# Kernel optimization log

Hardware: AMD Instinct MI355X
Metric: run time of the kernel (lower is better)

The kernel has to match this reference:

```python
import jax, jax.numpy as jnp
import numpy as np

B_SZ, SEQ = 1, 2048
D_MODEL, D_STATE, D_CONV, EXPAND = 768, 64, 4, 2
D_INNER = EXPAND * D_MODEL            # 1536
HEADDIM = 64
NHEADS = D_INNER // HEADDIM           # 24
CONV_DIM = D_INNER + 2 * D_STATE      # 1664
D_IN_PROJ = 2 * D_INNER + 2 * D_STATE + NHEADS  # 3224
HIDDEN = ((D_MODEL * EXPAND + 127) // 128) * 128  # 1536
EPS = 1e-5


def _ln(x, w, b):
    m = x.mean(-1, keepdims=True)
    v = ((x - m) ** 2).mean(-1, keepdims=True)
    return (x - m) * jax.lax.rsqrt(v + EPS) * w + b


def setup_inputs() -> dict:
    key = jax.random.key(0)
    ks = jax.random.split(key, 8)
    s = 0.02
    return {
        "x": jax.random.normal(ks[0], (B_SZ, SEQ, D_MODEL), jnp.float32),
        "ln1_w": jnp.ones((D_MODEL,), jnp.float32),
        "ln1_b": jnp.zeros((D_MODEL,), jnp.float32),
        "ln2_w": jnp.ones((D_MODEL,), jnp.float32),
        "ln2_b": jnp.zeros((D_MODEL,), jnp.float32),
        "in_proj_w": jax.random.normal(ks[1], (D_IN_PROJ, D_MODEL), jnp.float32) * s,
        "conv_w": jax.random.normal(ks[2], (CONV_DIM, D_CONV), jnp.float32) * s,
        "conv_b": jnp.zeros((CONV_DIM,), jnp.float32),
        "dt_bias": jax.random.normal(ks[3], (NHEADS,), jnp.float32) * 0.1,
        "A_log": jnp.log(jax.random.uniform(ks[4], (NHEADS,), jnp.float32, 1.0, 16.0)),
        "D_skip": jnp.ones((NHEADS,), jnp.float32),
        "ssm_norm_w": jnp.ones((D_INNER,), jnp.float32),
        "out_proj_w": jax.random.normal(ks[5], (D_MODEL, D_INNER), jnp.float32) * s,
        "fc1_w": jax.random.normal(ks[6], (2 * HIDDEN, D_MODEL), jnp.float32) * s,
        "fc2_w": jax.random.normal(ks[7], (D_MODEL, HIDDEN), jnp.float32) * s,
    }


def _block(x, ln1_w, ln1_b, ln2_w, ln2_b, in_proj_w, conv_w, conv_b,
           dt_bias, A_log, D_skip, ssm_norm_w, out_proj_w, fc1_w, fc2_w):
    Bb, L, _ = x.shape
    # --- Mamba2 SSM mixer ---
    h = _ln(x, ln1_w, ln1_b)
    zxbcdt = jnp.einsum('bld,pd->blp', h, in_proj_w)  # (B,L,D_IN_PROJ)
    z = zxbcdt[..., :D_INNER]
    xBC = zxbcdt[..., D_INNER:D_INNER + CONV_DIM]
    dt = zxbcdt[..., D_INNER + CONV_DIM:]             # (B,L,NHEADS)
    # causal depthwise conv1d (kernel D_CONV)
    xp = jnp.pad(xBC, ((0, 0), (D_CONV - 1, 0), (0, 0)))
    xBC = sum(xp[:, k:k + L, :] * conv_w[:, k] for k in range(D_CONV)) + conv_b
    xBC = jax.nn.silu(xBC)
    xs = xBC[..., :D_INNER].reshape(Bb, L, NHEADS, HEADDIM)
    Bm = xBC[..., D_INNER:D_INNER + D_STATE]          # (B,L,N) ngroups=1
    Cm = xBC[..., D_INNER + D_STATE:]                 # (B,L,N)
    dt = jax.nn.softplus(dt + dt_bias)                # (B,L,H)
    dA = jnp.exp(dt * (-jnp.exp(A_log)))              # (B,L,H)
    dtx = dt[..., None] * xs                          # (B,L,H,P)

    def step(hprev, inp):
        dA_t, dtx_t, B_t, C_t = inp
        hn = hprev * dA_t[:, :, None, None] + dtx_t[..., None] * B_t[:, None, None, :]
        return hn, jnp.einsum('bhps,bs->bhp', hn, C_t)

    h0 = jnp.zeros((Bb, NHEADS, HEADDIM, D_STATE), x.dtype)
    _, ys = jax.lax.scan(step, h0, (dA.swapaxes(0, 1), dtx.swapaxes(0, 1),
                                    Bm.swapaxes(0, 1), Cm.swapaxes(0, 1)))
    y = ys.swapaxes(0, 1) + D_skip[None, None, :, None] * xs  # (B,L,H,P)
    y = y.reshape(Bb, L, D_INNER) * jax.nn.silu(z)
    # gated RMSNorm
    y = y * jax.lax.rsqrt((y * y).mean(-1, keepdims=True) + EPS) * ssm_norm_w
    x = x + jnp.einsum('bli,di->bld', y, out_proj_w)
    # --- Gated MLP ---
    h2 = _ln(x, ln2_w, ln2_b)
    f = jnp.einsum('bld,hd->blh', h2, fc1_w)
    f = f[..., :HIDDEN] * jax.nn.silu(f[..., HIDDEN:])
    return x + jnp.einsum('blh,dh->bld', f, fc2_w)


def reference(x, ln1_w, ln1_b, ln2_w, ln2_b, in_proj_w, conv_w, conv_b,
              dt_bias, A_log, D_skip, ssm_norm_w, out_proj_w, fc1_w, fc2_w):
    return _block(x, ln1_w, ln1_b, ln2_w, ln2_b, in_proj_w, conv_w, conv_b,
                  dt_bias, A_log, D_skip, ssm_norm_w, out_proj_w, fc1_w, fc2_w)
```

## Files before the change

### kernel.cpp

```cpp
#include <hip/hip_runtime.h>
#include <math.h>

#define D_MODEL 768
#define SEQ 2048
#define D_STATE 64
#define D_CONV 4
#define D_INNER 1536
#define HEADDIM 64
#define NHEADS 24
#define CONV_DIM 1664
#define D_IN_PROJ 3224
#define HIDDEN 1536
#define EPS 1e-5f
#define NCHUNK 32
#define CHUNK 64

typedef short s16x8 __attribute__((ext_vector_type(8)));
typedef float f32x4 __attribute__((ext_vector_type(4)));

#define SWZ(row, k) (((row) << 6) + ((((k) >> 3) ^ ((row) & 7)) << 3) + ((k) & 7))

__device__ __forceinline__ float silu_f(float x) { return x / (1.f + expf(-x)); }

__device__ __forceinline__ short f2bf(float x) {
  unsigned u = __builtin_bit_cast(unsigned, x);
  unsigned r = (u + 0x7fffu + ((u >> 16) & 1u)) >> 16;
  return (short)r;
}
__device__ __forceinline__ float bf2f(short s) {
  unsigned u = ((unsigned)(unsigned short)s) << 16;
  return __builtin_bit_cast(float, u);
}

__device__ __forceinline__ float block_sum256(float v, float* sdata) {
#pragma unroll
  for (int o = 32; o > 0; o >>= 1) v += __shfl_down(v, o);
  int lane = threadIdx.x & 63, wid = threadIdx.x >> 6;
  __syncthreads();
  if (lane == 0) sdata[wid] = v;
  __syncthreads();
  if (threadIdx.x == 0) sdata[0] = sdata[0] + sdata[1] + sdata[2] + sdata[3];
  __syncthreads();
  return sdata[0];
}

__device__ __forceinline__ void gll16(const short* gsrc, const short* ldst) {
  __builtin_amdgcn_global_load_lds(
      (const __attribute__((address_space(1))) unsigned int*)(unsigned long long)gsrc,
      (__attribute__((address_space(3))) unsigned int*)(unsigned int)(unsigned long long)ldst,
      16, 0, 0);
}

__device__ __forceinline__ void ln_row(const float* __restrict__ xr,
                                       const float* __restrict__ w,
                                       const float* __restrict__ b,
                                       short* __restrict__ orow, float* red) {
  float v[3];
#pragma unroll
  for (int k = 0; k < 3; k++) v[k] = xr[threadIdx.x + k * 256];
  float s = v[0] + v[1] + v[2];
  s = block_sum256(s, red);
  float mean = s * (1.f / 768.f);
  float q = 0.f;
#pragma unroll
  for (int k = 0; k < 3; k++) { float d = v[k] - mean; q += d * d; }
  q = block_sum256(q, red);
  float rstd = rsqrtf(q * (1.f / 768.f) + EPS);
#pragma unroll
  for (int k = 0; k < 3; k++) {
    int i = threadIdx.x + k * 256;
    orow[i] = f2bf((v[k] - mean) * rstd * w[i] + b[i]);
  }
}

__global__ __launch_bounds__(256) void ln_kernel(const float* __restrict__ x,
                                                 const float* __restrict__ w,
                                                 const float* __restrict__ b,
                                                 short* __restrict__ out) {
  __shared__ float red[8];
  int row = blockIdx.x;
  ln_row(x + (size_t)row * D_MODEL, w, b, out + (size_t)row * D_MODEL, red);
}

#define T_WINP (3328 * 768)
#define R_WINP (3224 * 768)
#define T_FC1 (3072 * 768)
#define T_W768 (1536 * 768)
__global__ __launch_bounds__(256) void cast_ln_kernel(
    const float* __restrict__ x, const float* __restrict__ ln1w,
    const float* __restrict__ ln1b, short* __restrict__ hbf,
    const float* __restrict__ Win, const float* __restrict__ Wfc1,
    const float* __restrict__ Wout, const float* __restrict__ Wfc2,
    short* __restrict__ WA, short* __restrict__ WF1,
    short* __restrict__ WB, short* __restrict__ WC) {
  __shared__ float red[8];
  if (blockIdx.x < SEQ) {
    int row = blockIdx.x;
    ln_row(x + (size_t)row * D_MODEL, ln1w, ln1b, hbf + (size_t)row * D_MODEL, red);
    return;
  }
  int idx = (blockIdx.x - SEQ) * 256 + threadIdx.x;
  if (idx < T_WINP) {
    WA[idx] = (idx < R_WINP) ? f2bf(Win[idx]) : (short)0;
    return;
  }
  idx -= T_WINP;
  if (idx < T_FC1) {
    int np = idx / 768, k = idx % 768;
    int srow = (np & 1) ? (HIDDEN + (np >> 1)) : (np >> 1);
    WF1[idx] = f2bf(Wfc1[(size_t)srow * 768 + k]);
    return;
  }
  idx -= T_FC1;
  if (idx < T_W768) { WB[idx] = f2bf(Wout[idx]); return; }
  idx -= T_W768;
  if (idx < T_W768) WC[idx] = f2bf(Wfc2[idx]);
}

template <int MREP, int NREP, int CHUNKMODE, int OMODE>
__global__ __launch_bounds__(256) void mfma_gemm_bt(const short* __restrict__ A,
                                                    const short* __restrict__ Bw,
                                                    void* __restrict__ Cout,
                                                    const float* __restrict__ res,
                                                    int GX, int GY, int Nreal, int K) {
  constexpr int BMr = MREP * 32;
  constexpr int BNr = NREP * 32;
  __shared__ short As[BMr * 64];
  __shared__ short Bs[BNr * 64];
  int tid = threadIdx.x, w = tid >> 6, l = tid & 63;
  int per8 = gridDim.x >> 3;
  int L = (blockIdx.x & 7) * per8 + (blockIdx.x >> 3);
  int xt, yt;
  if constexpr (CHUNKMODE == 0) { xt = L / GY; yt = L - xt * GY; }
  else                          { yt = L / GX; xt = L - yt * GX; }
  int m0 = yt * BMr, n0 = xt * BNr;
  int wr = (w >> 1) * (MREP * 16), wc = (w & 1) * (NREP * 16);
  f32x4 acc[MREP][NREP] = {};

  for (int kt = 0; kt < K; kt += 64) {
    __syncthreads();
#pragma unroll
    for (int q = 0; q < BMr / 32; q++) {
      int chunk = w * (BMr / 32) + q;
      int rr = chunk * 8 + (l >> 3);
      int gs = (l & 7) ^ (rr & 7);
      gll16(A + (size_t)(m0 + rr) * K + kt + gs * 8, As + chunk * 512);
    }
#pragma unroll
    for (int q = 0; q < BNr / 32; q++) {
      int chunk = w * (BNr / 32) + q;
      int rr = chunk * 8 + (l >> 3);
      int gs = (l & 7) ^ (rr & 7);
      gll16(Bw + (size_t)(n0 + rr) * K + kt + gs * 8, Bs + chunk * 512);
    }
    __syncthreads();
#pragma unroll
    for (int half = 0; half < 2; half++) {
      s16x8 af[MREP], bfr[NREP];
      int kk = half * 32 + (l >> 4) * 8;
#pragma unroll
      for (int mi = 0; mi < MREP; mi++)
        af[mi] = *(const s16x8*)&As[SWZ(wr + mi * 16 + (l & 15), kk)];
#pragma unroll
      for (int nj = 0; nj < NREP; nj++)
        bfr[nj] = *(const s16x8*)&Bs[SWZ(wc + nj * 16 + (l & 15), kk)];
#pragma unroll
      for (int mi = 0; mi < MREP; mi++)
#pragma unroll
        for (int nj = 0; nj < NREP; nj++)
          acc[mi][nj] = __builtin_amdgcn_mfma_f32_16x16x32_bf16(af[mi], bfr[nj],
                                                                acc[mi][nj], 0, 0, 0);
    }
  }
#pragma unroll
  for (int mi = 0; mi < MREP; mi++)
#pragma unroll
    for (int nj = 0; nj < NREP; nj++)
#pragma unroll
      for (int r = 0; r < 4; r++) {
        int mm = m0 + wr + mi * 16 + (l >> 4) * 4 + r;
        int nn = n0 + wc + nj * 16 + (l & 15);
        float v = acc[mi][nj][r];
        if constexpr (OMODE == 0) {
          float* C = (float*)Cout;
          if (nn < Nreal) {
            if (res) v += res[(size_t)mm * Nreal + nn];
            C[(size_t)mm * Nreal + nn] = v;
          }
        } else if constexpr (OMODE == 1) {
          short* C = (short*)Cout;
          if (nn < Nreal) C[(size_t)mm * Nreal + nn] = f2bf(v);
        } else {
          float pv = __shfl_xor(v, 1);
          if ((l & 1) == 0) {
            short* g = (short*)Cout;
            g[(size_t)mm * (Nreal >> 1) + (nn >> 1)] = f2bf(v * silu_f(pv));
          }
        }
      }
}

__global__ __launch_bounds__(256) void conv_pack_kernel(const short* __restrict__ zx,
                                                        const float* __restrict__ cw,
                                                        const float* __restrict__ cb,
                                                        const float* __restrict__ dtb,
                                                        const float* __restrict__ Alog,
                                                        short* __restrict__ xsb,
                                                        short* __restrict__ XTall,
                                                        short* __restrict__ BTg,
                                                        short* __restrict__ BCbf,
                                                        float* __restrict__ dts,
                                                        float* __restrict__ laB) {
  int ct = blockIdx.x, rt = blockIdx.y;
  if (ct == 26) {
    int wv = threadIdx.x >> 6, t = threadIdx.x & 63;
    int gt = rt * 64 + t;
#pragma unroll
    for (int i = 0; i < 6; i++) {
      int h = wv * 6 + i;
      float xv = bf2f(zx[(size_t)gt * D_IN_PROJ + 3200 + h]) + dtb[h];
      float sp = (xv > 20.f) ? xv : log1pf(expf(xv));
      float la = -expf(Alog[h]) * sp;
#pragma unroll
      for (int off = 1; off < 64; off <<= 1) {
        float u = __shfl_up(la, off);
        if (t >= off) la += u;
      }
      dts[gt * NHEADS + h] = sp;
      laB[gt * NHEADS + h] = la;
    }
    return;
  }
  __shared__ float T[64][65];
  int lane = threadIdx.x & 63, grp = threadIdx.x >> 6;
  int c = ct * 64 + lane;
  float4 w4 = *(const float4*)&cw[c * 4];
  float cbv = cb[c];
  int t0 = rt * 64 + grp * 16;
  float vbuf[19];
#pragma unroll
  for (int jj = 0; jj < 19; jj++) {
    int tt = t0 + jj - 3;
    vbuf[jj] = (tt >= 0) ? bf2f(zx[(size_t)tt * D_IN_PROJ + D_INNER + c]) : 0.f;
  }
#pragma unroll
  for (int j = 0; j < 16; j++) {
    float acc = cbv + vbuf[j] * w4.x + vbuf[j + 1] * w4.y +
                vbuf[j + 2] * w4.z + vbuf[j + 3] * w4.w;
    float v = silu_f(acc);
    int row = grp * 16 + j;
    T[row][lane] = v;
    if (ct < 24)
      xsb[(size_t)(rt * 64 + row) * D_INNER + c] = f2bf(v);
    else
      BCbf[(size_t)(rt * 64 + row) * 128 + (ct - 24) * 64 + lane] = f2bf(v);
  }
  __syncthreads();
  if (ct < 24) {
#pragma unroll
    for (int j = 0; j < 16; j++) {
      int cc = grp * 16 + j;
      XTall[(size_t)(ct * 64 + cc) * 2048 + rt * 64 + lane] = f2bf(T[lane][cc]);
    }
  } else if (ct == 24) {
#pragma unroll
    for (int j = 0; j < 16; j++) {
      int cc = grp * 16 + j;
      BTg[(size_t)cc * 2048 + rt * 64 + lane] = f2bf(T[lane][cc]);
    }
  }
}

__global__ __launch_bounds__(256) void ssd_a_kernel(const short* __restrict__ BCbf,
                                                    const short* __restrict__ XTall,
                                                    const short* __restrict__ BTg,
                                                    const float* __restrict__ laB,
                                                    const float* __restrict__ dts,
                                                    short* __restrict__ ylg,
                                                    short* __restrict__ Sbh) {
  __shared__ short Cl[4096], Bl[4096], XTl[4096], BTl[4096], Ml[4096];
  __shared__ float la_s[64], dt_s[64], w_s[64];
  int b = blockIdx.x;
  int c = b / NHEADS, h = b % NHEADS;
  int tid = threadIdx.x, w = tid >> 6, l = tid & 63;

  {
    const short* gC = BCbf + (size_t)(c * 64) * 128 + 64;
    const short* gB = BCbf + (size_t)(c * 64) * 128;
    const short* gX = XTall + (size_t)(h * 64) * 2048 + c * 64;
    const short* gT = BTg + c * 64;
#pragma unroll
    for (int q = 0; q < 2; q++) {
      int row = w * 16 + q * 8 + (l >> 3);
      int ks = (l & 7) ^ (row & 7);
      int lofs = (w * 16 + q * 8) * 64;
      gll16(gC + (size_t)row * 128 + ks * 8, Cl + lofs);
      gll16(gB + (size_t)row * 128 + ks * 8, Bl + lofs);
      gll16(gX + (size_t)row * 2048 + ks * 8, XTl + lofs);
      gll16(gT + (size_t)row * 2048 + ks * 8, BTl + lofs);
    }
  }
  if (tid < 64) {
    la_s[tid] = laB[(c * CHUNK + tid) * NHEADS + h];
    dt_s[tid] = dts[(c * CHUNK + tid) * NHEADS + h];
  }
  __syncthreads();

  f32x4 gacc[4] = {};
#pragma unroll
  for (int kt = 0; kt < 2; kt++) {
    int ar = w * 16 + (l & 15);
    int kk = kt * 32 + (l >> 4) * 8;
    s16x8 af = *(const s16x8*)&Cl[SWZ(ar, kk)];
#pragma unroll
    for (int nj = 0; nj < 4; nj++) {
      s16x8 bf_ = *(const s16x8*)&Bl[SWZ(nj * 16 + (l & 15), kk)];
      gacc[nj] = __builtin_amdgcn_mfma_f32_16x16x32_bf16(af, bf_, gacc[nj], 0, 0, 0);
    }
  }
  if (tid < 64) w_s[tid] = __expf(la_s[63] - la_s[tid]) * dt_s[tid];
#pragma unroll
  for (int nj = 0; nj < 4; nj++)
#pragma unroll
    for (int r = 0; r < 4; r++) {
      int t = w * 16 + (l >> 4) * 4 + r;
      int s = nj * 16 + (l & 15);
      float m = (s <= t) ? gacc[nj][r] * __expf(la_s[t] - la_s[s]) * dt_s[s] : 0.f;
      Ml[SWZ(t, s)] = f2bf(m);
    }
  __syncthreads();
  {
    int s = tid & 63, tg = (tid >> 6) * 16;
#pragma unroll
    for (int j = 0; j < 16; j++) {
      int t = tg + j;
      int a = SWZ(s, t);
      BTl[a] = f2bf(bf2f(BTl[a]) * w_s[t]);
    }
  }
  __syncthreads();

  f32x4 yacc[4] = {};
#pragma unroll
  for (int kt = 0; kt < 2; kt++) {
    int ar = w * 16 + (l & 15);
    int kk = kt * 32 + (l >> 4) * 8;
    s16x8 af = *(const s16x8*)&Ml[SWZ(ar, kk)];
#pragma unroll
    for (int nj = 0; nj < 4; nj++) {
      s16x8 bf_ = *(const s16x8*)&XTl[SWZ(nj * 16 + (l & 15), kk)];
      yacc[nj] = __builtin_amdgcn_mfma_f32_16x16x32_bf16(af, bf_, yacc[nj], 0, 0, 0);
    }
  }
  f32x4 hacc[4] = {};
#pragma unroll
  for (int kt = 0; kt < 2; kt++) {
    int ar = w * 16 + (l & 15);
    int kk = kt * 32 + (l >> 4) * 8;
    s16x8 af = *(const s16x8*)&XTl[SWZ(ar, kk)];
#pragma unroll
    for (int nj = 0; nj < 4; nj++) {
      s16x8 bf_ = *(const s16x8*)&BTl[SWZ(nj * 16 + (l & 15), kk)];
      hacc[nj] = __builtin_amdgcn_mfma_f32_16x16x32_bf16(af, bf_, hacc[nj], 0, 0, 0);
    }
  }
#pragma unroll
  for (int nj = 0; nj < 4; nj++)
#pragma unroll
    for (int r = 0; r < 4; r++) {
      int t = w * 16 + (l >> 4) * 4 + r;
      int p = nj * 16 + (l & 15);
      ylg[(size_t)(c * CHUNK + t) * D_INNER + h * 64 + p] = f2bf(yacc[nj][r]);
      Sbh[((size_t)(c * NHEADS + h) * 64 + t) * 64 + p] = f2bf(hacc[nj][r]);
    }
}

__global__ __launch_bounds__(256) void scan2_kernel(const short* __restrict__ Sbh,
                                                    const float* __restrict__ laB,
                                                    short* __restrict__ Hsbf) {
  int idx = blockIdx.x * 256 + threadIdx.x;
  int hh = idx >> 12;
  int rem = idx & 4095;
  float Sv[NCHUNK];
#pragma unroll
  for (int c = 0; c < NCHUNK; c++)
    Sv[c] = bf2f(Sbh[((size_t)c * NHEADS + hh) * 4096 + rem]);
  float run = 0.f;
#pragma unroll
  for (int c = 0; c < NCHUNK; c++) {
    float P = __expf(laB[(c * CHUNK + CHUNK - 1) * NHEADS + hh]);
    Hsbf[((size_t)c * NHEADS + hh) * 4096 + rem] = f2bf(run);
    run = fmaf(P, run, Sv[c]);
  }
}

__global__ __launch_bounds__(256) void ssd_b_kernel(const short* __restrict__ BCbf,
                                                    const short* __restrict__ Hsbf,
                                                    const float* __restrict__ laB,
                                                    const float* __restrict__ Dsk,
                                                    const short* __restrict__ xsb,
                                                    const short* __restrict__ zx,
                                                    short* __restrict__ ylg) {
  __shared__ short Cl[4096], Hl[4096];
  __shared__ float la_s[64];
  int b = blockIdx.x;
  int c = b / NHEADS, h = b % NHEADS;
  int tid = threadIdx.x, w = tid >> 6, l = tid & 63;
  {
    const short* gC = BCbf + (size_t)(c * 64) * 128 + 64;
    const short* gH = Hsbf + (size_t)(c * NHEADS + h) * 4096;
#pragma unroll
    for (int q = 0; q < 2; q++) {
      int row = w * 16 + q * 8 + (l >> 3);
      int ks = (l & 7) ^ (row & 7);
      int lofs = (w * 16 + q * 8) * 64;
      gll16(gC + (size_t)row * 128 + ks * 8, Cl + lofs);
      gll16(gH + (size_t)row * 64 + ks * 8, Hl + lofs);
    }
  }
  if (tid < 64) la_s[tid] = laB[(c * CHUNK + tid) * NHEADS + h];
  __syncthreads();
  f32x4 acc[4] = {};
#pragma unroll
  for (int kt = 0; kt < 2; kt++) {
    int ar = w * 16 + (l & 15);
    int kk = kt * 32 + (l >> 4) * 8;
    s16x8 af = *(const s16x8*)&Cl[SWZ(ar, kk)];
#pragma unroll
    for (int nj = 0; nj < 4; nj++) {
      s16x8 bf_ = *(const s16x8*)&Hl[SWZ(nj * 16 + (l & 15), kk)];
      acc[nj] = __builtin_amdgcn_mfma_f32_16x16x32_bf16(af, bf_, acc[nj], 0, 0, 0);
    }
  }
  float Dv = Dsk[h];
#pragma unroll
  for (int nj = 0; nj < 4; nj++)
#pragma unroll
    for (int r = 0; r < 4; r++) {
      int t = w * 16 + (l >> 4) * 4 + r;
      int p = nj * 16 + (l & 15);
      size_t gt = c * CHUNK + t;
      size_t gi = gt * D_INNER + h * 64 + p;
      float yv = bf2f(ylg[gi]) + acc[nj][r] * __expf(la_s[t]) +
                 Dv * bf2f(xsb[gt * D_INNER + h * 64 + p]);
      float z = bf2f(zx[gt * D_IN_PROJ + h * 64 + p]);
      ylg[gi] = f2bf(yv * silu_f(z));
    }
}

__global__ __launch_bounds__(256) void rmsnorm_bf_kernel(const short* __restrict__ g,
                                                         const float* __restrict__ nw,
                                                         short* __restrict__ ybn) {
  __shared__ float red[8];
  int t = blockIdx.x;
  const short* gr = g + (size_t)t * D_INNER;
  float v[6];
  float ss = 0.f;
#pragma unroll
  for (int k = 0; k < 6; k++) {
    v[k] = bf2f(gr[threadIdx.x + k * 256]);
    ss += v[k] * v[k];
  }
  ss = block_sum256(ss, red);
  float rs = rsqrtf(ss * (1.f / (float)D_INNER) + EPS);
  short* orow = ybn + (size_t)t * D_INNER;
#pragma unroll
  for (int k = 0; k < 6; k++) {
    int i = threadIdx.x + k * 256;
    orow[i] = f2bf(v[k] * rs * nw[i]);
  }
}

extern "C" void kernel_launch(void* const* d_in, const int* in_sizes, int n_in,
                              void* d_out, int out_size, void* d_ws, size_t ws_size,
                              hipStream_t stream) {
  const float* x     = (const float*)d_in[0];
  const float* ln1w  = (const float*)d_in[1];
  const float* ln1b  = (const float*)d_in[2];
  const float* ln2w  = (const float*)d_in[3];
  const float* ln2b  = (const float*)d_in[4];
  const float* Win   = (const float*)d_in[5];
  const float* convw = (const float*)d_in[6];
  const float* convb = (const float*)d_in[7];
  const float* dtb   = (const float*)d_in[8];
  const float* Alog  = (const float*)d_in[9];
  const float* Dsk   = (const float*)d_in[10];
  const float* nrmw  = (const float*)d_in[11];
  const float* Wout  = (const float*)d_in[12];
  const float* Wfc1  = (const float*)d_in[13];
  const float* Wfc2  = (const float*)d_in[14];
  float* out = (float*)d_out;

  short* zxb   = (short*)d_ws;
  short* xsb   = zxb + 6602752;
  short* ylg   = xsb + 3145728;
  float* Sbf   = (float*)(ylg + 3145728);
  float* dts   = Sbf + 3145728;
  float* laB   = dts + 49152;
  short* hbf   = (short*)(laB + 49152);
  short* WA    = hbf + 1572864;
  short* WF1   = WA + 2555904;
  short* WB    = WF1 + 2359296;
  short* WC    = WB + 1179648;
  short* XTall = WC + 1179648;
  short* BTg   = XTall + 3145728;
  short* BCbf  = BTg + 131072;

  short* Sbh  = (short*)Sbf;
  short* Hsbf = XTall;
  float* x1   = Sbf;
  short* ybn  = (short*)(Sbf + 1572864);
  short* gbf  = zxb;

  cast_ln_kernel<<<SEQ + (T_WINP + T_FC1 + 2 * T_W768 + 255) / 256, 256, 0, stream>>>(
      x, ln1w, ln1b, hbf, Win, Wfc1, Wout, Wfc2, WA, WF1, WB, WC);
  mfma_gemm_bt<4, 4, 0, 1><<<26 * 16, 256, 0, stream>>>(hbf, WA, zxb, nullptr,
                                                        26, 16, D_IN_PROJ, D_MODEL);
  conv_pack_kernel<<<dim3(27, 32), 256, 0, stream>>>(zxb, convw, convb, dtb, Alog,
                                                     xsb, XTall, BTg, BCbf, dts, laB);
  ssd_a_kernel<<<NCHUNK * NHEADS, 256, 0, stream>>>(BCbf, XTall, BTg, laB, dts, ylg, Sbh);
  scan2_kernel<<<(NHEADS * 4096) / 256, 256, 0, stream>>>(Sbh, laB, Hsbf);
  ssd_b_kernel<<<NCHUNK * NHEADS, 256, 0, stream>>>(BCbf, Hsbf, laB, Dsk, xsb, zxb, ylg);
  rmsnorm_bf_kernel<<<SEQ, 256, 0, stream>>>(ylg, nrmw, ybn);
  mfma_gemm_bt<2, 2, 1, 0><<<12 * 32, 256, 0, stream>>>(ybn, WB, x1, x,
                                                        12, 32, D_MODEL, D_INNER);
  ln_kernel<<<SEQ, 256, 0, stream>>>(x1, ln2w, ln2b, hbf);
  mfma_gemm_bt<4, 4, 0, 2><<<24 * 16, 256, 0, stream>>>(hbf, WF1, gbf, nullptr,
                                                        24, 16, 2 * HIDDEN, D_MODEL);
  mfma_gemm_bt<2, 2, 1, 0><<<12 * 32, 256, 0, stream>>>(gbf, WC, out, x1,
                                                        12, 32, D_MODEL, HIDDEN);
}
```

Before: 154.5 us.

## Fold gated RMSNorm into ssd_b partial sums and out_proj GEMM epilogue

Removes the standalone rmsnorm kernel. ssd_b now writes per-head partial sums of squares, the norm weight is folded into the bf16 out_proj weight during the cast, and the out_proj GEMM computes a per-row rsqrt scale and applies it in its epilogue. This saves one launch and a full read and write of the 2048x1536 activation. In exchange the GEMM consumes unnormalized bf16 activations, which slightly changes rounding, and the ssqp buffer reuses the dts workspace.

```diff
diff --git a/kernel.cpp b/kernel.cpp
--- a/kernel.cpp
+++ b/kernel.cpp
@@ -91,6 +91,7 @@
     const float* __restrict__ ln1b, short* __restrict__ hbf,
     const float* __restrict__ Win, const float* __restrict__ Wfc1,
     const float* __restrict__ Wout, const float* __restrict__ Wfc2,
+    const float* __restrict__ nrmw,
     short* __restrict__ WA, short* __restrict__ WF1,
     short* __restrict__ WB, short* __restrict__ WC) {
   __shared__ float red[8];
@@ -112,7 +113,10 @@
     return;
   }
   idx -= T_FC1;
-  if (idx < T_W768) { WB[idx] = f2bf(Wout[idx]); return; }
+  if (idx < T_W768) {
+    WB[idx] = f2bf(Wout[idx] * nrmw[idx % D_INNER]);
+    return;
+  }
   idx -= T_W768;
   if (idx < T_W768) WC[idx] = f2bf(Wfc2[idx]);
 }
@@ -122,11 +126,13 @@
                                                     const short* __restrict__ Bw,
                                                     void* __restrict__ Cout,
                                                     const float* __restrict__ res,
+                                                    const float* __restrict__ ssqp,
                                                     int GX, int GY, int Nreal, int K) {
   constexpr int BMr = MREP * 32;
   constexpr int BNr = NREP * 32;
   __shared__ short As[BMr * 64];
   __shared__ short Bs[BNr * 64];
+  __shared__ float rs_s[BMr];
   int tid = threadIdx.x, w = tid >> 6, l = tid & 63;
   int per8 = gridDim.x >> 3;
   int L = (blockIdx.x & 7) * per8 + (blockIdx.x >> 3);
@@ -137,6 +143,16 @@
   int wr = (w >> 1) * (MREP * 16), wc = (w & 1) * (NREP * 16);
   f32x4 acc[MREP][NREP] = {};
 
+  if constexpr (OMODE == 3) {
+    if (tid < BMr) {
+      const float* sp = ssqp + (size_t)(m0 + tid) * NHEADS;
+      float s = 0.f;
+#pragma unroll
+      for (int i = 0; i < NHEADS; i++) s += sp[i];
+      rs_s[tid] = rsqrtf(s * (1.f / (float)D_INNER) + EPS);
+    }
+  }
+
   for (int kt = 0; kt < K; kt += 64) {
     __syncthreads();
 #pragma unroll
@@ -178,7 +194,8 @@
     for (int nj = 0; nj < NREP; nj++)
 #pragma unroll
       for (int r = 0; r < 4; r++) {
-        int mm = m0 + wr + mi * 16 + (l >> 4) * 4 + r;
+        int lr = wr + mi * 16 + (l >> 4) * 4 + r;
+        int mm = m0 + lr;
         int nn = n0 + wc + nj * 16 + (l & 15);
         float v = acc[mi][nj][r];
         if constexpr (OMODE == 0) {
@@ -190,11 +207,17 @@
         } else if constexpr (OMODE == 1) {
           short* C = (short*)Cout;
           if (nn < Nreal) C[(size_t)mm * Nreal + nn] = f2bf(v);
-        } else {
+        } else if constexpr (OMODE == 2) {
           float pv = __shfl_xor(v, 1);
           if ((l & 1) == 0) {
             short* g = (short*)Cout;
             g[(size_t)mm * (Nreal >> 1) + (nn >> 1)] = f2bf(v * silu_f(pv));
+          }
+        } else {
+          float* C = (float*)Cout;
+          if (nn < Nreal) {
+            v = v * rs_s[lr] + res[(size_t)mm * Nreal + nn];
+            C[(size_t)mm * Nreal + nn] = v;
           }
         }
       }
@@ -400,7 +423,8 @@
                                                     const float* __restrict__ Dsk,
                                                     const short* __restrict__ xsb,
                                                     const short* __restrict__ zx,
-                                                    short* __restrict__ ylg) {
+                                                    short* __restrict__ ylg,
+                                                    float* __restrict__ ssqp) {
   __shared__ short Cl[4096], Hl[4096];
   __shared__ float la_s[64];
   int b = blockIdx.x;
@@ -433,6 +457,7 @@
     }
   }
   float Dv = Dsk[h];
+  float sq[4] = {0.f, 0.f, 0.f, 0.f};
 #pragma unroll
   for (int nj = 0; nj < 4; nj++)
 #pragma unroll
@@ -444,30 +469,20 @@
       float yv = bf2f(ylg[gi]) + acc[nj][r] * __expf(la_s[t]) +
                  Dv * bf2f(xsb[gt * D_INNER + h * 64 + p]);
       float z = bf2f(zx[gt * D_IN_PROJ + h * 64 + p]);
-      ylg[gi] = f2bf(yv * silu_f(z));
-    }
-}
-
-__global__ __launch_bounds__(256) void rmsnorm_bf_kernel(const short* __restrict__ g,
-                                                         const float* __restrict__ nw,
-                                                         short* __restrict__ ybn) {
-  __shared__ float red[8];
-  int t = blockIdx.x;
-  const short* gr = g + (size_t)t * D_INNER;
-  float v[6];
-  float ss = 0.f;
-#pragma unroll
-  for (int k = 0; k < 6; k++) {
-    v[k] = bf2f(gr[threadIdx.x + k * 256]);
-    ss += v[k] * v[k];
-  }
-  ss = block_sum256(ss, red);
-  float rs = rsqrtf(ss * (1.f / (float)D_INNER) + EPS);
-  short* orow = ybn + (size_t)t * D_INNER;
-#pragma unroll
-  for (int k = 0; k < 6; k++) {
-    int i = threadIdx.x + k * 256;
-    orow[i] = f2bf(v[k] * rs * nw[i]);
+      short gb = f2bf(yv * silu_f(z));
+      ylg[gi] = gb;
+      float gf = bf2f(gb);
+      sq[r] += gf * gf;
+    }
+#pragma unroll
+  for (int r = 0; r < 4; r++) {
+    float s = sq[r];
+    s += __shfl_xor(s, 1); s += __shfl_xor(s, 2);
+    s += __shfl_xor(s, 4); s += __shfl_xor(s, 8);
+    if ((l & 15) == 0) {
+      int t = w * 16 + (l >> 4) * 4 + r;
+      ssqp[(size_t)(c * CHUNK + t) * NHEADS + h] = s;
+    }
   }
 }
 
@@ -509,24 +524,23 @@
   short* Sbh  = (short*)Sbf;
   short* Hsbf = XTall;
   float* x1   = Sbf;
-  short* ybn  = (short*)(Sbf + 1572864);
+  float* ssqp = dts;
   short* gbf  = zxb;
 
   cast_ln_kernel<<<SEQ + (T_WINP + T_FC1 + 2 * T_W768 + 255) / 256, 256, 0, stream>>>(
-      x, ln1w, ln1b, hbf, Win, Wfc1, Wout, Wfc2, WA, WF1, WB, WC);
-  mfma_gemm_bt<4, 4, 0, 1><<<26 * 16, 256, 0, stream>>>(hbf, WA, zxb, nullptr,
+      x, ln1w, ln1b, hbf, Win, Wfc1, Wout, Wfc2, nrmw, WA, WF1, WB, WC);
+  mfma_gemm_bt<4, 4, 0, 1><<<26 * 16, 256, 0, stream>>>(hbf, WA, zxb, nullptr, nullptr,
                                                         26, 16, D_IN_PROJ, D_MODEL);
   conv_pack_kernel<<<dim3(27, 32), 256, 0, stream>>>(zxb, convw, convb, dtb, Alog,
                                                      xsb, XTall, BTg, BCbf, dts, laB);
   ssd_a_kernel<<<NCHUNK * NHEADS, 256, 0, stream>>>(BCbf, XTall, BTg, laB, dts, ylg, Sbh);
   scan2_kernel<<<(NHEADS * 4096) / 256, 256, 0, stream>>>(Sbh, laB, Hsbf);
-  ssd_b_kernel<<<NCHUNK * NHEADS, 256, 0, stream>>>(BCbf, Hsbf, laB, Dsk, xsb, zxb, ylg);
-  rmsnorm_bf_kernel<<<SEQ, 256, 0, stream>>>(ylg, nrmw, ybn);
-  mfma_gemm_bt<2, 2, 1, 0><<<12 * 32, 256, 0, stream>>>(ybn, WB, x1, x,
+  ssd_b_kernel<<<NCHUNK * NHEADS, 256, 0, stream>>>(BCbf, Hsbf, laB, Dsk, xsb, zxb, ylg, ssqp);
+  mfma_gemm_bt<2, 2, 1, 3><<<12 * 32, 256, 0, stream>>>(ylg, WB, x1, x, ssqp,
                                                         12, 32, D_MODEL, D_INNER);
   ln_kernel<<<SEQ, 256, 0, stream>>>(x1, ln2w, ln2b, hbf);
-  mfma_gemm_bt<4, 4, 0, 2><<<24 * 16, 256, 0, stream>>>(hbf, WF1, gbf, nullptr,
+  mfma_gemm_bt<4, 4, 0, 2><<<24 * 16, 256, 0, stream>>>(hbf, WF1, gbf, nullptr, nullptr,
                                                         24, 16, 2 * HIDDEN, D_MODEL);
-  mfma_gemm_bt<2, 2, 1, 0><<<12 * 32, 256, 0, stream>>>(gbf, WC, out, x1,
+  mfma_gemm_bt<2, 2, 1, 0><<<12 * 32, 256, 0, stream>>>(gbf, WC, out, x1, nullptr,
                                                         12, 32, D_MODEL, HIDDEN);
 }
```

Result: faster. 151.4 us (-2.1%).
